# Performance work log

Measured on AMD Instinct MI355X. Metric: run time of the kernel, lower is better.

The kernel has to match this reference:

```python
import jax, jax.numpy as jnp
import numpy as np

_EPS = 1e-5
_I48 = float(1.0 / np.sqrt(48.0))
_I16 = float(1.0 / np.sqrt(16.0))
# fully-connected TP paths (mul_in, mul_out) for hidden(48x0e+48x1o+16x1e) x sh(0e+1e+2e) -> hidden
_PATHS = [(48, 48), (48, 16), (48, 48), (48, 48), (48, 48), (16, 16), (16, 48), (16, 16), (16, 16)]
_NW = sum(i * o for i, o in _PATHS)  # 11520


def _ln(x, g, b):
    mu = x.mean(-1, keepdims=True)
    var = ((x - mu) ** 2).mean(-1, keepdims=True)
    return g * (x - mu) * jax.lax.rsqrt(var + _EPS) + b


def _split(W):
    out, off = [], 0
    for i, o in _PATHS:
        out.append(W[:, off:off + i * o].reshape(-1, i, o))
        off += i * o
    return out


def _forward(protein_coords, protein_features, ligand_coords, ligand_features, t,
             te_w1, te_b1, te_w2, te_b2, te_ln_g, te_ln_b,
             pe_w1, pe_b1, pe_ln_g, pe_ln_b, pe_w2, pe_b2,
             le_w1, le_b1, le_ln_g, le_ln_b, le_w2, le_b2,
             sp_w, sp_b, emb_w, ee_w1, ee_b1, ee_w2, ee_b2,
             conv_w1, conv_b1, conv_w2, conv_b2, conv_w3, conv_b3,
             bn_gs, bn_bs, bn_gv, bn_gw, si_ws, si_wv, si_ww,
             out_ws, out_wv, edge_src, edge_dst):
    Nl = ligand_coords.shape[0]
    Np = protein_coords.shape[0]
    N = Nl + Np
    E = edge_src.shape[0]
    silu = jax.nn.silu

    # sinusoidal time embedding -> Linear/SiLU/Linear/LayerNorm
    half = 32
    freq = jnp.exp(jnp.arange(half, dtype=jnp.float32) * (-np.log(10000.0) / (half - 1)))
    emb = t[:, None] * freq[None, :]
    emb = jnp.concatenate([jnp.sin(emb), jnp.cos(emb)], -1)  # (1, 64)
    temb = _ln(silu(emb @ te_w1 + te_b1) @ te_w2 + te_b2, te_ln_g, te_ln_b)

    # scalar node encoders (dropout = eval identity)
    protein_ca = protein_coords[:, 0, :]
    ph = silu(_ln(protein_features @ pe_w1 + pe_b1, pe_ln_g, pe_ln_b)) @ pe_w2 + pe_b2
    lh = silu(_ln(ligand_features @ le_w1 + le_b1, le_ln_g, le_ln_b)) @ le_w2 + le_b2

    # edge geometry (ligand -> protein) + spherical harmonics in Cartesian form
    vec = ligand_coords[edge_src] - protein_ca[edge_dst]  # (E, 3)
    dist = jnp.sqrt((vec ** 2).sum(-1) + 1e-12)
    n = vec / dist[:, None]  # unit vector = l=1 SH
    Q = n[:, :, None] * n[:, None, :] - jnp.eye(3, dtype=n.dtype) / 3.0  # l=2 SH (traceless sym)
    te_exp = jnp.broadcast_to(temb[0], (E, temb.shape[-1]))
    ef = silu(jnp.concatenate([dist[:, None], te_exp], -1) @ ee_w1 + ee_b1) @ ee_w2 + ee_b2  # (E, 32)

    # input embedding: scalars only feed 0e; 1o/1e channels start at zero
    comb = jnp.concatenate([lh, ph], 0) @ sp_w + sp_b  # (N, 48)
    s = (comb @ emb_w) * _I48
    v = jnp.zeros((N, 48, 3), s.dtype)
    w = jnp.zeros((N, 16, 3), s.dtype)

    dst_n = edge_dst + Nl
    deg = jax.ops.segment_sum(jnp.ones((E,), s.dtype), dst_n, N).clip(1.0)

    for i in range(conv_w1.shape[0]):
        # edge MLP -> per-edge fully-connected tensor-product weights
        m = silu(ef @ conv_w1[i] + conv_b1[i])
        m = silu(m @ conv_w2[i] + conv_b2[i])
        Wt = m @ conv_w3[i] + conv_b3[i]  # (E, 11520)
        Wss, Wsw, Wv0, Wv1, Wv2, Ww0, Wws, Ww1, Ww2 = _split(Wt)

        se, ve, we = s[edge_src], v[edge_src], w[edge_src]
        wn = jnp.einsum('eid,ed->ei', we, n)        # 1e x 1e -> 0e (dot)
        cv = jnp.cross(ve, n[:, None, :])           # 1o x 1e -> 1o (cross)
        cw = jnp.cross(we, n[:, None, :])           # 1e x 1e -> 1e (cross)
        qv = jnp.einsum('edc,eic->eid', Q, ve)      # 1o x 2e -> 1o
        qw = jnp.einsum('edc,eic->eid', Q, we)      # 1e x 2e -> 1e

        m_s = jnp.einsum('eio,ei->eo', Wss, se) * _I48 + jnp.einsum('eio,ei->eo', Wws, wn) * _I16
        m_v = (jnp.einsum('eio,eid->eod', Wv0, ve) + jnp.einsum('eio,eid->eod', Wv1, cv)
               + jnp.einsum('eio,eid->eod', Wv2, qv)) * _I48
        m_w = jnp.einsum('eio,ei,ed->eod', Wsw, se, n) * _I48 + (
            jnp.einsum('eio,eid->eod', Ww0, we) + jnp.einsum('eio,eid->eod', Ww1, cw)
            + jnp.einsum('eio,eid->eod', Ww2, qw)) * _I16

        # scatter-mean to destination nodes
        S = jax.ops.segment_sum(m_s, dst_n, N) / deg[:, None]
        V = jax.ops.segment_sum(m_v, dst_n, N) / deg[:, None, None]
        Wm = jax.ops.segment_sum(m_w, dst_n, N) / deg[:, None, None]

        # self interaction (per-irrep linear)
        a_s = S + (s @ si_ws[i]) * _I48
        a_v = V + jnp.einsum('io,nid->nod', si_wv[i], v) * _I48
        a_w = Wm + jnp.einsum('io,nid->nod', si_ww[i], w) * _I16

        # equivariant batch norm (batch statistics)
        mu = a_s.mean(0)
        var = ((a_s - mu) ** 2).mean(0)
        n_s = bn_gs[i] * (a_s - mu) * jax.lax.rsqrt(var + _EPS) + bn_bs[i]
        n_v = a_v * (bn_gv[i] * jax.lax.rsqrt((a_v ** 2).sum(-1).mean(0) + _EPS))[None, :, None]
        n_w = a_w * (bn_gw[i] * jax.lax.rsqrt((a_w ** 2).sum(-1).mean(0) + _EPS))[None, :, None]

        s, v, w = s + n_s, v + n_v, w + n_w

    feats = (s[:Nl] @ out_ws) * _I48                          # (Nl, 256)
    out_v = jnp.einsum('io,nid->nod', out_wv, v[:Nl]) * _I48  # (Nl, 3, 3)
    vf = out_v.mean(1)                                        # vector_field (Nl, 3)
    return jnp.concatenate([vf, feats], -1)                   # (Nl, 259)


def setup_inputs():
    key = jax.random.key(0)
    ks = iter(jax.random.split(key, 80))
    f32 = jnp.float32

    def nrm(shape, scale=1.0):
        return jax.random.normal(next(ks), shape, f32) * scale

    def lin(fi, fo, lead=()):
        return nrm(lead + (fi, fo), 1.0 / np.sqrt(fi)), jnp.zeros(lead + (fo,), f32)

    Nl, Np, E, L = 2048, 4096, 8192, 6
    inp = {}
    inp['protein_coords'] = nrm((Np, 2, 3), 5.0)
    inp['protein_features'] = nrm((Np, 96))
    inp['ligand_coords'] = nrm((Nl, 3), 5.0)
    inp['ligand_features'] = nrm((Nl, 52))
    inp['t'] = jax.random.uniform(next(ks), (1,), f32)
    inp['te_w1'], inp['te_b1'] = lin(64, 128)
    inp['te_w2'], inp['te_b2'] = lin(128, 64)
    inp['te_ln_g'], inp['te_ln_b'] = jnp.ones((64,), f32), jnp.zeros((64,), f32)
    inp['pe_w1'], inp['pe_b1'] = lin(96, 128)
    inp['pe_ln_g'], inp['pe_ln_b'] = jnp.ones((128,), f32), jnp.zeros((128,), f32)
    inp['pe_w2'], inp['pe_b2'] = lin(128, 48)
    inp['le_w1'], inp['le_b1'] = lin(52, 128)
    inp['le_ln_g'], inp['le_ln_b'] = jnp.ones((128,), f32), jnp.zeros((128,), f32)
    inp['le_w2'], inp['le_b2'] = lin(128, 48)
    inp['sp_w'], inp['sp_b'] = lin(48, 48)
    inp['emb_w'] = nrm((48, 48))
    inp['ee_w1'], inp['ee_b1'] = lin(65, 32)
    inp['ee_w2'], inp['ee_b2'] = lin(32, 32)
    inp['conv_w1'], inp['conv_b1'] = lin(32, 128, (L,))
    inp['conv_w2'], inp['conv_b2'] = lin(128, 128, (L,))
    inp['conv_w3'], inp['conv_b3'] = lin(128, _NW, (L,))
    inp['bn_gs'], inp['bn_bs'] = jnp.ones((L, 48), f32), jnp.zeros((L, 48), f32)
    inp['bn_gv'], inp['bn_gw'] = jnp.ones((L, 48), f32), jnp.ones((L, 16), f32)
    inp['si_ws'] = nrm((L, 48, 48))
    inp['si_wv'] = nrm((L, 48, 48))
    inp['si_ww'] = nrm((L, 16, 16))
    inp['out_ws'] = nrm((48, 256))
    inp['out_wv'] = nrm((48, 3))
    inp['edge_src'] = jax.random.randint(next(ks), (E,), 0, Nl)
    inp['edge_dst'] = jax.random.randint(next(ks), (E,), 0, Np)
    return inp


def reference(protein_coords, protein_features, ligand_coords, ligand_features, t,
              te_w1, te_b1, te_w2, te_b2, te_ln_g, te_ln_b,
              pe_w1, pe_b1, pe_ln_g, pe_ln_b, pe_w2, pe_b2,
              le_w1, le_b1, le_ln_g, le_ln_b, le_w2, le_b2,
              sp_w, sp_b, emb_w, ee_w1, ee_b1, ee_w2, ee_b2,
              conv_w1, conv_b1, conv_w2, conv_b2, conv_w3, conv_b3,
              bn_gs, bn_bs, bn_gv, bn_gw, si_ws, si_wv, si_ww,
              out_ws, out_wv, edge_src, edge_dst):
    return _forward(protein_coords, protein_features, ligand_coords, ligand_features, t,
                    te_w1, te_b1, te_w2, te_b2, te_ln_g, te_ln_b,
                    pe_w1, pe_b1, pe_ln_g, pe_ln_b, pe_w2, pe_b2,
                    le_w1, le_b1, le_ln_g, le_ln_b, le_w2, le_b2,
                    sp_w, sp_b, emb_w, ee_w1, ee_b1, ee_w2, ee_b2,
                    conv_w1, conv_b1, conv_w2, conv_b2, conv_w3, conv_b3,
                    bn_gs, bn_bs, bn_gv, bn_gw, si_ws, si_wv, si_ww,
                    out_ws, out_wv, edge_src, edge_dst)
```

## Files before the change

kernel.cpp:

```cpp
#include <hip/hip_runtime.h>
#include <hip/hip_bf16.h>
#include <math.h>

#define I48 0.14433756729740643f
#define NKB 194
#define KCH 4
#define KSPL 6

typedef __attribute__((ext_vector_type(8))) _Float16 half8;
typedef __attribute__((ext_vector_type(4))) float f32x4;

__device__ __forceinline__ float silu_f(float x){ return x / (1.f + __expf(-x)); }

__global__ void k_temb(const float* __restrict__ t_in,
                       const float* __restrict__ w1, const float* __restrict__ b1,
                       const float* __restrict__ w2, const float* __restrict__ b2,
                       const float* __restrict__ g,  const float* __restrict__ b,
                       float* __restrict__ temb){
  __shared__ float emb[64], h1[128], red[128];
  __shared__ float s_mu, s_rs;
  int t = threadIdx.x;
  float tv = t_in[0];
  if (t < 64){
    int i = t & 31;
    float fr = __expf((float)i * (-9.210340371976184f/31.f));
    float a = tv * fr;
    emb[t] = (t < 32) ? sinf(a) : cosf(a);
  }
  __syncthreads();
  {
    float z = b1[t];
    for (int i=0;i<64;i++) z += emb[i]*w1[i*128+t];
    h1[t] = silu_f(z);
  }
  __syncthreads();
  float tp = 0.f;
  if (t < 64){
    tp = b2[t];
    for (int j=0;j<128;j++) tp += h1[j]*w2[j*64+t];
  }
  red[t] = (t<64)? tp : 0.f;
  __syncthreads();
  for (int st=64;st;st>>=1){ if(t<st) red[t]+=red[t+st]; __syncthreads(); }
  if (t==0) s_mu = red[0]/64.f;
  __syncthreads();
  float d = tp - s_mu;
  red[t] = (t<64)? d*d : 0.f;
  __syncthreads();
  for (int st=64;st;st>>=1){ if(t<st) red[t]+=red[t+st]; __syncthreads(); }
  if (t==0) s_rs = rsqrtf(red[0]/64.f + 1e-5f);
  __syncthreads();
  if (t<64) temb[t] = g[t]*(d*s_rs) + b[t];
}

__global__ void k_encall(const float* __restrict__ pf, const float* __restrict__ lf, int Nl,
    const float* __restrict__ pw1, const float* __restrict__ pb1,
    const float* __restrict__ pg,  const float* __restrict__ pbb,
    const float* __restrict__ pw2, const float* __restrict__ pb2,
    const float* __restrict__ lw1, const float* __restrict__ lb1,
    const float* __restrict__ lg,  const float* __restrict__ lbb,
    const float* __restrict__ lw2, const float* __restrict__ lb2,
    const float* __restrict__ spw, const float* __restrict__ spb,
    const float* __restrict__ embw, float* __restrict__ s){
  __shared__ float sx[96], sh[128], red[128], vout[48], c48[48];
  __shared__ float s_mu, s_rs;
  int row = blockIdx.x, t = threadIdx.x;
  bool lig = row < Nl;
  int in_dim = lig ? 52 : 96;
  const float* x  = lig ? (lf + (size_t)row*52) : (pf + (size_t)(row-Nl)*96);
  const float* w1 = lig ? lw1 : pw1;
  const float* b1 = lig ? lb1 : pb1;
  const float* g  = lig ? lg  : pg;
  const float* bb = lig ? lbb : pbb;
  const float* w2 = lig ? lw2 : pw2;
  const float* b2 = lig ? lb2 : pb2;
  for (int i=t;i<in_dim;i+=128) sx[i] = x[i];
  __syncthreads();
  float z = b1[t];
  for (int i=0;i<in_dim;i++) z += sx[i]*w1[i*128+t];
  red[t]=z; __syncthreads();
  for (int st=64;st;st>>=1){ if(t<st) red[t]+=red[t+st]; __syncthreads(); }
  if(!t) s_mu = red[0]/128.f;
  __syncthreads();
  float d = z - s_mu;
  red[t]=d*d; __syncthreads();
  for (int st=64;st;st>>=1){ if(t<st) red[t]+=red[t+st]; __syncthreads(); }
  if(!t) s_rs = rsqrtf(red[0]/128.f+1e-5f);
  __syncthreads();
  float h = g[t]*(d*s_rs)+bb[t];
  sh[t] = silu_f(h);
  __syncthreads();
  if (t<48){
    float o = b2[t];
    for (int j=0;j<128;j++) o += sh[j]*w2[j*48+t];
    vout[t] = o;
  }
  __syncthreads();
  if (t<48){
    float c = spb[t];
    for (int i=0;i<48;i++) c += vout[i]*spw[i*48+t];
    c48[t] = c;
  }
  __syncthreads();
  if (t<48){
    float v = 0.f;
    for (int i=0;i<48;i++) v += c48[i]*embw[i*48+t];
    s[(size_t)row*48+t] = v*I48;
  }
}

__global__ void k_edge(const float* __restrict__ lc, const float* __restrict__ pc,
                       const int* __restrict__ src, const int* __restrict__ dst,
                       const float* __restrict__ temb,
                       const float* __restrict__ w1, const float* __restrict__ b1,
                       const float* __restrict__ w2, const float* __restrict__ b2,
                       float* __restrict__ ef, float* __restrict__ degf,
                       int E, int Nl){
  __shared__ float sh_h[2][32];
  int t = threadIdx.x, sub = t>>5, j = t&31;
  int e = blockIdx.x*2 + sub;
  if (e < E){
    int s_ = src[e], d_ = dst[e];
    float vx = lc[(size_t)s_*3+0]-pc[(size_t)d_*6+0];
    float vy = lc[(size_t)s_*3+1]-pc[(size_t)d_*6+1];
    float vz = lc[(size_t)s_*3+2]-pc[(size_t)d_*6+2];
    float dist = sqrtf(vx*vx+vy*vy+vz*vz+1e-12f);
    float h = b1[j] + dist*w1[j];
    for (int a=0;a<64;a++) h += temb[a]*w1[(a+1)*32+j];
    sh_h[sub][j] = silu_f(h);
  }
  __syncthreads();
  if (e < E){
    float o = b2[j];
    for (int a=0;a<32;a++) o += sh_h[sub][a]*w2[a*32+j];
    ef[(size_t)e*32+j] = o;
    if (j==0) atomicAdd(&degf[Nl + dst[e]], 1.f);
  }
}

__global__ __launch_bounds__(256) void k_pack2(
    const float* __restrict__ w3, const float* __restrict__ b3,
    const float* __restrict__ w1, const float* __restrict__ w2,
    _Float16* __restrict__ wbh,
    _Float16* __restrict__ w1p, _Float16* __restrict__ w2p, int L){
  const int t = threadIdx.x;
  const int b = blockIdx.x;
  const int mainN = L*48;
  if (b < mainN){
    __shared__ float sw3[128][49];
    const int l = b / 48, i = b - (b/48)*48;
    const float* srow = w3 + (size_t)l*128*11520 + (size_t)i*48;
    for (int v = t; v < 1536; v += 256){
      int kk = v / 12, og = v - kk*12;
      float4 f = *(const float4*)(srow + (size_t)kk*11520 + og*4);
      sw3[kk][og*4+0] = f.x; sw3[kk][og*4+1] = f.y;
      sw3[kk][og*4+2] = f.z; sw3[kk][og*4+3] = f.w;
    }
    __syncthreads();
    _Float16* dst0 = wbh + ((size_t)(l*NKB + i*4))*1536;
    for (int v = t; v < 768; v += 256){
      int kb = v / 192, rem = v - kb*192;
      int nt = rem >> 6, lane = rem & 63;
      int kkb = kb*32 + ((lane>>4)<<3);
      int o = nt*16 + (lane & 15);
      half8 hv;
      #pragma unroll
      for (int j=0;j<8;j++) hv[j] = (_Float16)sw3[kkb + j][o];
      *(half8*)(dst0 + ((size_t)(kb*3 + nt))*512 + lane*8) = hv;
    }
    return;
  }
  if (b < mainN + L){
    const int l = b - mainN;
    _Float16* dst0 = wbh + ((size_t)l*NKB + 192)*1536;
    const float* b3l = b3 + (size_t)l*11520;
    for (int v = t; v < 384; v += 256){
      int kb = v / 192, rem = v - kb*192;
      int nt = rem >> 6, lane = rem & 63;
      int iib = kb*32 + ((lane>>4)<<3);
      int o = nt*16 + (lane & 15);
      half8 hv;
      #pragma unroll
      for (int j=0;j<8;j++){
        int ii = iib + j;
        hv[j] = (ii < 48) ? (_Float16)b3l[ii*48 + o] : (_Float16)0.f;
      }
      *(half8*)(dst0 + ((size_t)(kb*3 + nt))*512 + lane*8) = hv;
    }
    return;
  }
  if (b < mainN + 2*L){
    const int l = b - mainN - L;
    for (int v = t; v < 512; v += 256){
      int nt = v >> 6, lane = v & 63;
      int kbse = (lane>>4)<<3;
      int o = nt*16 + (lane & 15);
      half8 hv;
      #pragma unroll
      for (int j=0;j<8;j++) hv[j] = (_Float16)w1[((size_t)l*32 + kbse + j)*128 + o];
      *(half8*)(w1p + (((size_t)l*8 + nt)*64 + lane)*8) = hv;
    }
    return;
  }
  {
    const int l = b - mainN - 2*L;
    for (int v = t; v < 2048; v += 256){
      int kb = v >> 9, rem = v & 511;
      int nt = rem >> 6, lane = rem & 63;
      int kbse = kb*32 + ((lane>>4)<<3);
      int o = nt*16 + (lane & 15);
      half8 hv;
      #pragma unroll
      for (int j=0;j<8;j++) hv[j] = (_Float16)w2[((size_t)l*128 + kbse + j)*128 + o];
      *(half8*)(w2p + (((size_t)(l*4 + kb)*8 + nt)*64 + lane)*8) = hv;
    }
    return;
  }
}

__global__ __launch_bounds__(256) void k_mlp2(
    const float* __restrict__ ef,
    const _Float16* __restrict__ w1p, const float* __restrict__ b1a,
    const _Float16* __restrict__ w2p, const float* __restrict__ b2a,
    _Float16* __restrict__ m2h, int E){
  __shared__ __align__(16) _Float16 sef[64][40];
  __shared__ __align__(16) _Float16 shh[64][136];
  __shared__ float sb1[128], sb2[128];
  const int t = threadIdx.x, lane = t & 63, w = t >> 6;
  const int e0 = blockIdx.x * 64;
  const int l  = blockIdx.y;
  const _Float16* w1l = w1p + (size_t)l*4096;
  const _Float16* w2l = w2p + (size_t)l*16384;
  if (t < 128) sb1[t] = b1a[l*128 + t];
  else         sb2[t-128] = b2a[l*128 + (t-128)];
  {
    int row = t >> 2, g = t & 3;
    const float* p = ef + ((size_t)(e0+row))*32 + g*8;
    float4 p0 = *(const float4*)p, p1 = *(const float4*)(p+4);
    half8 hv;
    hv[0]=(_Float16)p0.x; hv[1]=(_Float16)p0.y; hv[2]=(_Float16)p0.z; hv[3]=(_Float16)p0.w;
    hv[4]=(_Float16)p1.x; hv[5]=(_Float16)p1.y; hv[6]=(_Float16)p1.z; hv[7]=(_Float16)p1.w;
    *(half8*)&sef[row][g*8] = hv;
  }
  __syncthreads();
  const int m = lane & 15, quad = lane >> 4;
  const int r = w*16 + m;
  half8 a1 = *(const half8*)&sef[r][quad*8];
  f32x4 acc1[8];
  #pragma unroll
  for (int nt=0; nt<8; nt++){
    half8 b = *(const half8*)(w1l + (nt*64 + lane)*8);
    f32x4 z = {0.f,0.f,0.f,0.f};
    acc1[nt] = __builtin_amdgcn_mfma_f32_16x16x32_f16(a1, b, z, 0,0,0);
  }
  #pragma unroll
  for (int nt=0; nt<8; nt++){
    float bv = sb1[nt*16 + m];
    #pragma unroll
    for (int rr=0; rr<4; rr++)
      shh[w*16 + quad*4 + rr][nt*16 + m] = (_Float16)silu_f(acc1[nt][rr] + bv);
  }
  __syncthreads();
  f32x4 acc2[8];
  #pragma unroll
  for (int nt=0;nt<8;nt++) acc2[nt] = (f32x4){0.f,0.f,0.f,0.f};
  #pragma unroll
  for (int kb=0; kb<4; kb++){
    half8 a2 = *(const half8*)&shh[r][kb*32 + quad*8];
    #pragma unroll
    for (int nt=0; nt<8; nt++){
      half8 b = *(const half8*)(w2l + ((size_t)(kb*8+nt)*64 + lane)*8);
      acc2[nt] = __builtin_amdgcn_mfma_f32_16x16x32_f16(a2, b, acc2[nt], 0,0,0);
    }
  }
  __syncthreads();
  #pragma unroll
  for (int nt=0; nt<8; nt++){
    float bv = sb2[nt*16 + m];
    #pragma unroll
    for (int rr=0; rr<4; rr++)
      shh[w*16 + quad*4 + rr][nt*16 + m] = (_Float16)silu_f(acc2[nt][rr] + bv);
  }
  __syncthreads();
  for (int q = t; q < 64*16; q += 256){
    int row = q >> 4, c = q & 15;
    half8 hv = *(const half8*)&shh[row][c*8];
    *(half8*)(m2h + ((size_t)l*E + e0 + row)*128 + c*8) = hv;
  }
}

__global__ __launch_bounds__(256) void k_msg7(
    const _Float16* __restrict__ m2h, const float* __restrict__ s,
    const float* __restrict__ a_s, const float* __restrict__ bnlp,
    const float* __restrict__ gp, const float* __restrict__ bp, int apply, int N,
    const _Float16* __restrict__ wbh,
    const int* __restrict__ src, const int* __restrict__ dst,
    float* __restrict__ Sacc, int Nl){
  __shared__ __align__(16) _Float16 sB[2][KCH*1536];
  __shared__ __align__(16) _Float16 sseq[64][72];
  __shared__ int sdst[64];
  __shared__ float ksc[48], kbs[48];
  const int t = threadIdx.x, lane = t & 63, w = t >> 6;
  const int e0 = blockIdx.x * 64;
  const int by = blockIdx.y;
  const int kb0 = by*32;
  const int kb1 = (by==KSPL-1) ? NKB : kb0+32;

  if (t < 48){
    if (apply){
      float su = bnlp[t], sq = bnlp[48+t];
      float mu  = su/(float)N;
      float var = sq/(float)N - mu*mu;
      float r = rsqrtf(var + 1e-5f);
      float sc = gp[t]*r;
      ksc[t] = sc; kbs[t] = bp[t] - mu*sc;
    } else { ksc[t]=0.f; kbs[t]=0.f; }
  }
  if (t < 64) sdst[t] = dst[e0+t];
  __syncthreads();

  for (int q = t; q < 64*9; q += 256){
    int e = q/9, g = q - e*9;
    half8 hv = {};
    if (g < 6){
      size_t base = (size_t)src[e0+e]*48 + g*8;
      const float* sp = s + base;
      if (apply){
        const float* ap = a_s + base;
        #pragma unroll
        for (int j=0;j<8;j++){
          int o = g*8+j;
          hv[j] = (_Float16)(sp[j] + ap[j]*ksc[o] + kbs[o]);
        }
      } else {
        #pragma unroll
        for (int j=0;j<8;j++) hv[j] = (_Float16)sp[j];
      }
    }
    *(half8*)&sseq[e][g*8] = hv;
  }

  const int m = lane & 15, quad = lane >> 4;
  const int r0 = w*16 + m;

  half8 f0[4];
  {
    const _Float16* base0 = m2h + (size_t)(e0+r0)*128 + quad*8;
    #pragma unroll
    for (int sub=0; sub<4; sub++) f0[sub] = *(const half8*)(base0 + sub*32);
  }

  auto stage = [&](int c){
    int kbase = kb0 + c*KCH;
    int nk = kb1 - kbase; if (nk > KCH) nk = KCH;
    int bytes = nk*3072;
    const char* g = (const char*)wbh + (size_t)kbase*3072;
    char* lb = (char*)sB[c&1];
    for (int off = w*1024; off < bytes; off += 4096){
      __builtin_amdgcn_global_load_lds(
        (const __attribute__((address_space(1))) void*)(g + off + (size_t)lane*16),
        (__attribute__((address_space(3))) void*)(lb + off), 16, 0, 0);
    }
  };
  stage(0);

  f32x4 acc0={0.f,0.f,0.f,0.f}, acc1={0.f,0.f,0.f,0.f}, acc2={0.f,0.f,0.f,0.f};

  const int nch = (kb1-kb0+KCH-1)/KCH;
  for (int c = 0; c < nch; c++){
    __syncthreads();
    if (c+1 < nch) stage(c+1);
    int kbase = kb0 + c*KCH;
    int kbn = kb1 - kbase; if (kbn > KCH) kbn = KCH;
    const _Float16* bb = sB[c&1];
    if (kbn == KCH && kbase < 192){
      int i = kbase >> 2;
      _Float16 sv0 = sseq[r0][i];
      half8 s0v = {sv0,sv0,sv0,sv0,sv0,sv0,sv0,sv0};
      #pragma unroll
      for (int kk = 0; kk < KCH; kk++){
        half8 a0 = f0[kk] * s0v;
        const _Float16* bk = bb + kk*1536 + lane*8;
        half8 b0 = *(const half8*)(bk);
        half8 b1 = *(const half8*)(bk + 512);
        half8 b2 = *(const half8*)(bk + 1024);
        acc0 = __builtin_amdgcn_mfma_f32_16x16x32_f16(a0, b0, acc0, 0, 0, 0);
        acc1 = __builtin_amdgcn_mfma_f32_16x16x32_f16(a0, b1, acc1, 0, 0, 0);
        acc2 = __builtin_amdgcn_mfma_f32_16x16x32_f16(a0, b2, acc2, 0, 0, 0);
      }
    } else {
      for (int kk = 0; kk < kbn; kk++){
        int kblk = kbase + kk;
        int ib = ((kblk-192) << 5) + quad*8;
        half8 a0 = *(const half8*)&sseq[r0][ib];
        const _Float16* bk = bb + kk*1536 + lane*8;
        half8 b0 = *(const half8*)(bk);
        half8 b1 = *(const half8*)(bk + 512);
        half8 b2 = *(const half8*)(bk + 1024);
        acc0 = __builtin_amdgcn_mfma_f32_16x16x32_f16(a0, b0, acc0, 0, 0, 0);
        acc1 = __builtin_amdgcn_mfma_f32_16x16x32_f16(a0, b1, acc1, 0, 0, 0);
        acc2 = __builtin_amdgcn_mfma_f32_16x16x32_f16(a0, b2, acc2, 0, 0, 0);
      }
    }
  }
  #pragma unroll
  for (int r = 0; r < 4; r++){
    int el0 = w*16 + quad*4 + r;
    float* p0 = Sacc + (size_t)(Nl + sdst[el0])*48 + m;
    atomicAdd(p0 +  0, acc0[r]*I48);
    atomicAdd(p0 + 16, acc1[r]*I48);
    atomicAdd(p0 + 32, acc2[r]*I48);
  }
}

__global__ __launch_bounds__(256) void k_node3(float* __restrict__ Sacc,
                       const float* __restrict__ degf,
                       float* __restrict__ s, const float* __restrict__ siw,
                       float* __restrict__ a_s,
                       const float* __restrict__ bnlp, const float* __restrict__ gp,
                       const float* __restrict__ bp, int apply,
                       float* __restrict__ bnl, int N){
  __shared__ float sh_s[16][48];
  __shared__ float sw[2304];
  __shared__ float csum[48], csq[48];
  __shared__ float ksc[48], kbs[48];
  int t = threadIdx.x;
  int n0 = blockIdx.x*16;
  if (t < 48){
    if (apply){
      float su = bnlp[t], sq = bnlp[48+t];
      float mu  = su/(float)N;
      float var = sq/(float)N - mu*mu;
      float r = rsqrtf(var + 1e-5f);
      float sc = gp[t]*r;
      ksc[t] = sc; kbs[t] = bp[t] - mu*sc;
    } else { ksc[t]=0.f; kbs[t]=0.f; }
    csum[t]=0.f; csq[t]=0.f;
  }
  for (int q=t;q<2304;q+=256) sw[q] = siw[q];
  __syncthreads();
  for (int q=t;q<768;q+=256){
    int nl=q/48, o=q-nl*48;
    size_t idx = (size_t)(n0+nl)*48+o;
    float v = s[idx];
    if (apply){
      v += a_s[idx]*ksc[o] + kbs[o];
      s[idx] = v;
    }
    sh_s[nl][o] = v;
  }
  __syncthreads();
  int nl = t>>4;
  int ob = (t&15)*3;
  int n = n0+nl;
  float dg = degf[n]; if (dg < 1.f) dg = 1.f;
  float inv = 1.f/dg;
  #pragma unroll
  for (int j=0;j<3;j++){
    int o = ob+j;
    size_t idx = (size_t)n*48+o;
    float acc = 0.f;
    for (int i=0;i<48;i++) acc += sh_s[nl][i]*sw[i*48+o];
    float a = Sacc[idx]*inv + acc*I48;
    Sacc[idx] = 0.f;
    a_s[idx] = a;
    atomicAdd(&csum[o], a);
    atomicAdd(&csq[o], a*a);
  }
  __syncthreads();
  if (t<96) atomicAdd(&bnl[t], (t<48) ? csum[t] : csq[t-48]);
}

__global__ void k_out2(const float* __restrict__ s, const float* __restrict__ a_s,
                       const float* __restrict__ bnlp, const float* __restrict__ gp,
                       const float* __restrict__ bp, int N,
                       const float* __restrict__ ows, float* __restrict__ out){
  __shared__ float sh_s[48];
  __shared__ float ksc[48], kbs[48];
  int n = blockIdx.x, t = threadIdx.x;
  if (t < 48){
    float su = bnlp[t], sq = bnlp[48+t];
    float mu  = su/(float)N;
    float var = sq/(float)N - mu*mu;
    float r = rsqrtf(var + 1e-5f);
    float sc = gp[t]*r;
    ksc[t] = sc; kbs[t] = bp[t] - mu*sc;
  }
  __syncthreads();
  if (t<48){
    size_t idx = (size_t)n*48+t;
    sh_s[t] = s[idx] + a_s[idx]*ksc[t] + kbs[t];
  }
  __syncthreads();
  float acc = 0.f;
  for (int i=0;i<48;i++) acc += sh_s[i]*ows[i*256+t];
  out[(size_t)n*259 + 3 + t] = acc*I48;
  if (t<3) out[(size_t)n*259 + t] = 0.f;
}

extern "C" void kernel_launch(void* const* d_in, const int* in_sizes, int n_in,
                              void* d_out, int out_size, void* d_ws, size_t ws_size,
                              hipStream_t stream){
  const float* protein_coords   = (const float*)d_in[0];
  const float* protein_features = (const float*)d_in[1];
  const float* ligand_coords    = (const float*)d_in[2];
  const float* ligand_features  = (const float*)d_in[3];
  const float* t_in    = (const float*)d_in[4];
  const float* te_w1   = (const float*)d_in[5];
  const float* te_b1   = (const float*)d_in[6];
  const float* te_w2   = (const float*)d_in[7];
  const float* te_b2   = (const float*)d_in[8];
  const float* te_ln_g = (const float*)d_in[9];
  const float* te_ln_b = (const float*)d_in[10];
  const float* pe_w1   = (const float*)d_in[11];
  const float* pe_b1   = (const float*)d_in[12];
  const float* pe_ln_g = (const float*)d_in[13];
  const float* pe_ln_b = (const float*)d_in[14];
  const float* pe_w2   = (const float*)d_in[15];
  const float* pe_b2   = (const float*)d_in[16];
  const float* le_w1   = (const float*)d_in[17];
  const float* le_b1   = (const float*)d_in[18];
  const float* le_ln_g = (const float*)d_in[19];
  const float* le_ln_b = (const float*)d_in[20];
  const float* le_w2   = (const float*)d_in[21];
  const float* le_b2   = (const float*)d_in[22];
  const float* sp_w    = (const float*)d_in[23];
  const float* sp_b    = (const float*)d_in[24];
  const float* emb_w   = (const float*)d_in[25];
  const float* ee_w1   = (const float*)d_in[26];
  const float* ee_b1   = (const float*)d_in[27];
  const float* ee_w2   = (const float*)d_in[28];
  const float* ee_b2   = (const float*)d_in[29];
  const float* conv_w1 = (const float*)d_in[30];
  const float* conv_b1 = (const float*)d_in[31];
  const float* conv_w2 = (const float*)d_in[32];
  const float* conv_b2 = (const float*)d_in[33];
  const float* conv_w3 = (const float*)d_in[34];
  const float* conv_b3 = (const float*)d_in[35];
  const float* bn_gs   = (const float*)d_in[36];
  const float* bn_bs   = (const float*)d_in[37];
  const float* si_ws   = (const float*)d_in[40];
  const float* out_ws  = (const float*)d_in[43];
  const int* edge_src  = (const int*)d_in[45];
  const int* edge_dst  = (const int*)d_in[46];

  int Np = in_sizes[0]/6;
  int Nl = in_sizes[2]/3;
  int E  = in_sizes[45];
  int N  = Nl+Np;
  int L  = in_sizes[36]/48;

  float* W = (float*)d_ws;
  size_t off = 0;
  auto alloc = [&](size_t n)->float*{ float* p = W+off; off += (n+63)&~(size_t)63; return p; };
  float* degf  = alloc(N);
  float* Sacc  = alloc((size_t)N*48);
  float* bnb   = alloc((size_t)L*96);
  float* temb  = alloc(64);
  float* sbuf  = alloc((size_t)N*48);
  float* ef    = alloc((size_t)E*32);
  float* a_s   = alloc((size_t)N*48);
  _Float16* m2h = (_Float16*)alloc((size_t)L*E*128/2 + 64);
  _Float16* wbh = (_Float16*)alloc((size_t)L*NKB*1536/2 + 64);
  _Float16* w1p = (_Float16*)alloc((size_t)L*4096/2 + 64);
  _Float16* w2p = (_Float16*)alloc((size_t)L*16384/2 + 64);

  hipMemsetAsync(degf, 0, ((size_t)N + (size_t)N*48 + (size_t)L*96 + 192)*sizeof(float), stream);
  k_pack2<<<L*51,256,0,stream>>>(conv_w3, conv_b3, conv_w1, conv_w2, wbh, w1p, w2p, L);
  k_temb<<<1,128,0,stream>>>(t_in, te_w1, te_b1, te_w2, te_b2, te_ln_g, te_ln_b, temb);
  k_encall<<<N,128,0,stream>>>(protein_features, ligand_features, Nl,
                               pe_w1, pe_b1, pe_ln_g, pe_ln_b, pe_w2, pe_b2,
                               le_w1, le_b1, le_ln_g, le_ln_b, le_w2, le_b2,
                               sp_w, sp_b, emb_w, sbuf);
  k_edge<<<(E+1)/2,64,0,stream>>>(ligand_coords, protein_coords, edge_src, edge_dst, temb,
                                  ee_w1, ee_b1, ee_w2, ee_b2, ef, degf, E, Nl);
  dim3 mlpg(E/64, L);
  k_mlp2<<<mlpg,256,0,stream>>>(ef, w1p, conv_b1, w2p, conv_b2, m2h, E);

  dim3 mgrid(E/64, KSPL);
  for (int l=0;l<L;l++){
    const float* bnlp = (l>0) ? (bnb + (l-1)*96) : bnb;
    const float* gp   = (l>0) ? (bn_gs + (l-1)*48) : bn_gs;
    const float* bp   = (l>0) ? (bn_bs + (l-1)*48) : bn_bs;
    int apply = (l>0) ? 1 : 0;
    k_msg7<<<mgrid,256,0,stream>>>(m2h + (size_t)l*E*128, sbuf, a_s, bnlp, gp, bp, apply, N,
                                   wbh + (size_t)l*NKB*1536, edge_src, edge_dst, Sacc, Nl);
    k_node3<<<N/16,256,0,stream>>>(Sacc, degf, sbuf, si_ws + (size_t)l*2304, a_s,
                                   bnlp, gp, bp, apply, bnb + l*96, N);
  }
  k_out2<<<Nl,256,0,stream>>>(sbuf, a_s, bnb + (L-1)*96, bn_gs + (L-1)*48, bn_bs + (L-1)*48,
                              N, out_ws, (float*)d_out);
}
```

Baseline: 447.0 us.

## Fuse per-layer message/node loop into one cooperative persistent kernel

Merges the per-layer message, node-update and output kernels into a single cooperative kernel that uses grid-wide syncs between phases instead of separate launches. This targets launch overhead and inter-kernel gaps across the layer loop. The cooperative kernel is capped at 3 blocks per CU and needs the whole grid co-resident, which can lower occupancy. If the cooperative launch fails it falls back to the old multi-launch path.

```diff
diff --git a/kernel.cpp b/kernel.cpp
--- a/kernel.cpp
+++ b/kernel.cpp
@@ -1,6 +1,9 @@
 #include <hip/hip_runtime.h>
+#include <hip/hip_cooperative_groups.h>
 #include <hip/hip_bf16.h>
 #include <math.h>
+
+namespace cg = cooperative_groups;
 
 #define I48 0.14433756729740643f
 #define NKB 194
@@ -289,7 +292,8 @@
   }
 }
 
-__global__ __launch_bounds__(256) void k_msg7(
+
+__device__ __forceinline__ void msg_body(int xe, int by,
     const _Float16* __restrict__ m2h, const float* __restrict__ s,
     const float* __restrict__ a_s, const float* __restrict__ bnlp,
     const float* __restrict__ gp, const float* __restrict__ bp, int apply, int N,
@@ -301,8 +305,7 @@
   __shared__ int sdst[64];
   __shared__ float ksc[48], kbs[48];
   const int t = threadIdx.x, lane = t & 63, w = t >> 6;
-  const int e0 = blockIdx.x * 64;
-  const int by = blockIdx.y;
+  const int e0 = xe * 64;
   const int kb0 = by*32;
   const int kb1 = (by==KSPL-1) ? NKB : kb0+32;
 
@@ -413,7 +416,7 @@
   }
 }
 
-__global__ __launch_bounds__(256) void k_node3(float* __restrict__ Sacc,
+__device__ __forceinline__ void node_body(int nb, float* __restrict__ Sacc,
                        const float* __restrict__ degf,
                        float* __restrict__ s, const float* __restrict__ siw,
                        float* __restrict__ a_s,
@@ -425,7 +428,7 @@
   __shared__ float csum[48], csq[48];
   __shared__ float ksc[48], kbs[48];
   int t = threadIdx.x;
-  int n0 = blockIdx.x*16;
+  int n0 = nb*16;
   if (t < 48){
     if (apply){
       float su = bnlp[t], sq = bnlp[48+t];
@@ -471,13 +474,14 @@
   if (t<96) atomicAdd(&bnl[t], (t<48) ? csum[t] : csq[t-48]);
 }
 
-__global__ void k_out2(const float* __restrict__ s, const float* __restrict__ a_s,
+__device__ __forceinline__ void out_body(int n, const float* __restrict__ s,
+                       const float* __restrict__ a_s,
                        const float* __restrict__ bnlp, const float* __restrict__ gp,
                        const float* __restrict__ bp, int N,
                        const float* __restrict__ ows, float* __restrict__ out){
   __shared__ float sh_s[48];
   __shared__ float ksc[48], kbs[48];
-  int n = blockIdx.x, t = threadIdx.x;
+  int t = threadIdx.x;
   if (t < 48){
     float su = bnlp[t], sq = bnlp[48+t];
     float mu  = su/(float)N;
@@ -496,6 +500,66 @@
   for (int i=0;i<48;i++) acc += sh_s[i]*ows[i*256+t];
   out[(size_t)n*259 + 3 + t] = acc*I48;
   if (t<3) out[(size_t)n*259 + t] = 0.f;
+  __syncthreads();
+}
+
+__global__ __launch_bounds__(256, 3) void k_loop(
+    const _Float16* __restrict__ m2h, float* __restrict__ s,
+    float* __restrict__ a_s, float* __restrict__ Sacc, float* __restrict__ bnb,
+    const float* __restrict__ bn_gs, const float* __restrict__ bn_bs,
+    const _Float16* __restrict__ wbh,
+    const int* __restrict__ src, const int* __restrict__ dst,
+    const float* __restrict__ degf, const float* __restrict__ si_ws,
+    const float* __restrict__ ows, float* __restrict__ out,
+    int E, int N, int Nl, int L){
+  cg::grid_group grid = cg::this_grid();
+  const int bid = blockIdx.x, nblk = gridDim.x;
+  const int NXB = E/64;
+  const int nnode = N/16;
+  for (int l = 0; l < L; l++){
+    const float* bnlp = (l>0) ? (bnb + (l-1)*96) : bnb;
+    const float* gp   = (l>0) ? (bn_gs + (l-1)*48) : bn_gs;
+    const float* bp   = (l>0) ? (bn_bs + (l-1)*48) : bn_bs;
+    int apply = (l>0) ? 1 : 0;
+    msg_body(bid % NXB, bid / NXB, m2h + (size_t)l*E*128, s, a_s, bnlp, gp, bp,
+             apply, N, wbh + (size_t)l*NKB*1536, src, dst, Sacc, Nl);
+    grid.sync();
+    if (bid < nnode)
+      node_body(bid, Sacc, degf, s, si_ws + (size_t)l*2304, a_s,
+                bnlp, gp, bp, apply, bnb + l*96, N);
+    grid.sync();
+  }
+  for (int n = bid; n < Nl; n += nblk)
+    out_body(n, s, a_s, bnb + (L-1)*96, bn_gs + (L-1)*48, bn_bs + (L-1)*48,
+             N, ows, out);
+}
+
+__global__ __launch_bounds__(256) void k_msg7(
+    const _Float16* __restrict__ m2h, const float* __restrict__ s,
+    const float* __restrict__ a_s, const float* __restrict__ bnlp,
+    const float* __restrict__ gp, const float* __restrict__ bp, int apply, int N,
+    const _Float16* __restrict__ wbh,
+    const int* __restrict__ src, const int* __restrict__ dst,
+    float* __restrict__ Sacc, int Nl){
+  msg_body(blockIdx.x, blockIdx.y, m2h, s, a_s, bnlp, gp, bp, apply, N,
+           wbh, src, dst, Sacc, Nl);
+}
+
+__global__ __launch_bounds__(256) void k_node3(float* __restrict__ Sacc,
+                       const float* __restrict__ degf,
+                       float* __restrict__ s, const float* __restrict__ siw,
+                       float* __restrict__ a_s,
+                       const float* __restrict__ bnlp, const float* __restrict__ gp,
+                       const float* __restrict__ bp, int apply,
+                       float* __restrict__ bnl, int N){
+  node_body(blockIdx.x, Sacc, degf, s, siw, a_s, bnlp, gp, bp, apply, bnl, N);
+}
+
+__global__ void k_out2(const float* __restrict__ s, const float* __restrict__ a_s,
+                       const float* __restrict__ bnlp, const float* __restrict__ gp,
+                       const float* __restrict__ bp, int N,
+                       const float* __restrict__ ows, float* __restrict__ out){
+  out_body(blockIdx.x, s, a_s, bnlp, gp, bp, N, ows, out);
 }
 
 extern "C" void kernel_launch(void* const* d_in, const int* in_sizes, int n_in,
@@ -577,17 +641,36 @@
   dim3 mlpg(E/64, L);
   k_mlp2<<<mlpg,256,0,stream>>>(ef, w1p, conv_b1, w2p, conv_b2, m2h, E);
 
-  dim3 mgrid(E/64, KSPL);
-  for (int l=0;l<L;l++){
-    const float* bnlp = (l>0) ? (bnb + (l-1)*96) : bnb;
-    const float* gp   = (l>0) ? (bn_gs + (l-1)*48) : bn_gs;
-    const float* bp   = (l>0) ? (bn_bs + (l-1)*48) : bn_bs;
-    int apply = (l>0) ? 1 : 0;
-    k_msg7<<<mgrid,256,0,stream>>>(m2h + (size_t)l*E*128, sbuf, a_s, bnlp, gp, bp, apply, N,
-                                   wbh + (size_t)l*NKB*1536, edge_src, edge_dst, Sacc, Nl);
-    k_node3<<<N/16,256,0,stream>>>(Sacc, degf, sbuf, si_ws + (size_t)l*2304, a_s,
-                                   bnlp, gp, bp, apply, bnb + l*96, N);
-  }
-  k_out2<<<Nl,256,0,stream>>>(sbuf, a_s, bnb + (L-1)*96, bn_gs + (L-1)*48, bn_bs + (L-1)*48,
-                              N, out_ws, (float*)d_out);
-}
+  int NXB  = E/64;
+  int nblk = NXB*KSPL;
+  bool coop = (nblk <= 768) && (E % 64 == 0) && (N % 16 == 0);
+
+  bool launched = false;
+  if (coop){
+    float* outp = (float*)d_out;
+    void* kargs[] = {
+      (void*)&m2h, (void*)&sbuf, (void*)&a_s, (void*)&Sacc, (void*)&bnb,
+      (void*)&bn_gs, (void*)&bn_bs, (void*)&wbh, (void*)&edge_src, (void*)&edge_dst,
+      (void*)&degf, (void*)&si_ws, (void*)&out_ws, (void*)&outp,
+      (void*)&E, (void*)&N, (void*)&Nl, (void*)&L };
+    hipError_t cerr = hipLaunchCooperativeKernel(reinterpret_cast<void*>(k_loop),
+        dim3(nblk), dim3(256), kargs, 0, stream);
+    launched = (cerr == hipSuccess);
+  }
+
+  if (!launched){
+    dim3 mgrid(NXB, KSPL);
+    for (int l=0;l<L;l++){
+      const float* bnlp = (l>0) ? (bnb + (l-1)*96) : bnb;
+      const float* gp   = (l>0) ? (bn_gs + (l-1)*48) : bn_gs;
+      const float* bp   = (l>0) ? (bn_bs + (l-1)*48) : bn_bs;
+      int apply = (l>0) ? 1 : 0;
+      k_msg7<<<mgrid,256,0,stream>>>(m2h + (size_t)l*E*128, sbuf, a_s, bnlp, gp, bp, apply, N,
+                                     wbh + (size_t)l*NKB*1536, edge_src, edge_dst, Sacc, Nl);
+      k_node3<<<N/16,256,0,stream>>>(Sacc, degf, sbuf, si_ws + (size_t)l*2304, a_s,
+                                     bnlp, gp, bp, apply, bnb + l*96, N);
+    }
+    k_out2<<<Nl,256,0,stream>>>(sbuf, a_s, bnb + (L-1)*96, bn_gs + (L-1)*48, bn_bs + (L-1)*48,
+                                N, out_ws, (float*)d_out);
+  }
+}
```

After: 1.416 ms. 3.17x slower.
